# Performance work log

Hardware: AMD Instinct MI355X
Metric: run time of the kernel (lower is better)

Reference implementation:

```python
import jax, jax.numpy as jnp
import numpy as np

EPS = float(np.finfo(np.float32).eps)
B, N, NUM_ATOM, K = 16, 256, 64, 20
NUM_EDGETYPE = 3
SHORT = (1, 2, 3)
LONG = (3, 5, 7)
HIDDEN = (128, 128)
OUT = 1
SCALES = len(SHORT) + len(LONG) + NUM_EDGETYPE + 1  # 10
LB = 1e-4  # lanczos breakdown tolerance


def _xavier(k, fi, fo):
    return jax.random.uniform(k, (fi, fo), jnp.float32, -1.0, 1.0) * (6.0 / (fi + fo)) ** 0.5


def setup_inputs() -> dict:
    key = jax.random.key(0)
    ks = jax.random.split(key, 12)
    inp = {}
    inp["node_feat"] = jax.random.randint(ks[0], (B, N), 0, NUM_ATOM)
    inp["L"] = jax.random.uniform(ks[1], (B, N, N, NUM_EDGETYPE + 1), jnp.float32)
    # embedding_map: Linear(num_atom,1024) -> ReLU -> Linear(1024,num_atom)
    inp["emb_w1"] = _xavier(ks[2], NUM_ATOM, 1024); inp["emb_b1"] = jnp.zeros((1024,), jnp.float32)
    inp["emb_w2"] = _xavier(ks[3], 1024, NUM_ATOM); inp["emb_b2"] = jnp.zeros((NUM_ATOM,), jnp.float32)
    # eigen_map per long scale: Linear(K*K,1024) -> ReLU -> Linear(1024,K*K)
    S, K2 = len(LONG), K * K
    inp["eig_w1"] = jnp.stack([_xavier(jax.random.fold_in(ks[4], i), K2, 1024) for i in range(S)])
    inp["eig_b1"] = jnp.zeros((S, 1024), jnp.float32)
    inp["eig_w2"] = jnp.stack([_xavier(jax.random.fold_in(ks[5], i), 1024, K2) for i in range(S)])
    inp["eig_b2"] = jnp.zeros((S, K2), jnp.float32)
    dims = [NUM_ATOM] + list(HIDDEN) + [OUT]
    inp["filt_w0"] = _xavier(ks[6], dims[0] * SCALES, dims[1]); inp["filt_b0"] = jnp.zeros((dims[1],), jnp.float32)
    inp["filt_w1"] = _xavier(ks[7], dims[1] * SCALES, dims[2]); inp["filt_b1"] = jnp.zeros((dims[2],), jnp.float32)
    inp["filt_wo"] = _xavier(ks[8], dims[2], dims[3]); inp["filt_bo"] = jnp.zeros((dims[3],), jnp.float32)
    inp["att_w"] = _xavier(ks[9], dims[2], 1); inp["att_b"] = jnp.zeros((1,), jnp.float32)
    return inp


def _graph_laplacian(feat, adj_mask):
    # feat: B x N x D; pairwise gaussian affinity, sym-normalized (alpha=0.5)
    diff = feat[:, :, None, :] - feat[:, None, :, :]           # B,N,N,D
    dist2 = jnp.sum(diff * diff, axis=-1).reshape(B, -1)       # B,N*N
    sigma2 = jnp.mean(dist2, axis=1, keepdims=True)
    A = jnp.exp(-dist2 / sigma2).reshape(B, N, N) * adj_mask
    row_sum = jnp.sum(A, axis=2, keepdims=True)
    pad = jnp.where(row_sum == 0.0, 1.0, 0.0)
    D = 1.0 / jnp.sqrt(row_sum + pad)
    return D * A * jnp.swapaxes(D, 1, 2)


def _lanczos(A, key):
    # sequential Lanczos tridiagonalization with double Gram-Schmidt reorth
    q = jax.random.normal(key, (B, N), jnp.float32)
    q = q / jnp.linalg.norm(q, axis=1, keepdims=True)

    def step(carry, i):
        Qbuf, q_prev, qc, beta_prev, valid = carry
        z = jnp.einsum('bij,bj->bi', A, qc)
        alpha = jnp.sum(qc * z, axis=1)
        z = z - alpha[:, None] * qc - beta_prev[:, None] * q_prev
        for _ in range(2):  # reorthogonalize against Q[1..ii-1] (zero cols are no-ops)
            coef = jnp.einsum('bnk,bn->bk', Qbuf, z) / (jnp.sum(Qbuf * Qbuf, axis=1) + EPS)
            z = z - jnp.einsum('bnk,bk->bn', Qbuf, coef)
        beta = jnp.sqrt(jnp.sum(z * z, axis=1))
        valid = valid * (beta >= LB).astype(jnp.float32)
        q_next = z * valid[:, None] / (beta[:, None] + EPS)
        Qbuf = Qbuf.at[:, :, i].set(qc)
        return (Qbuf, qc, q_next, beta, valid), (alpha, beta, valid, qc)

    init = (jnp.zeros((B, N, K), jnp.float32), jnp.zeros((B, N), jnp.float32), q,
            jnp.zeros((B,), jnp.float32), jnp.ones((B,), jnp.float32))
    _, (alphas, betas, valids, qs) = jax.lax.scan(step, init, jnp.arange(K))
    alpha = alphas.T            # B,K
    beta = betas.T              # B,K
    valid = valids.T            # B,K (cumulative 1..1 0..0)
    idx = jnp.sum(valid, axis=1).astype(jnp.int32)   # rank per sample
    alpha = alpha * valid
    beta = beta[:, :K - 1] * valid[:, :K - 1]
    T = jax.vmap(lambda a, b: jnp.diag(a) + jnp.diag(b, 1) + jnp.diag(b, -1))(alpha, beta)
    Q = jnp.transpose(qs, (1, 2, 0))  # B,N,K
    # faithful to source: zero node rows >= idx_mask (only when idx < N)
    row_ok = (jnp.arange(N)[None, :] < idx[:, None]) | (idx[:, None] >= N)
    Q = Q * valid[:, None, :] * row_ok[:, :, None].astype(jnp.float32)
    return T, Q


def _spectral_filters(T, Q, eig_w1, eig_b1, eig_w2, eig_b2, key):
    T_list = []
    TT = T
    b = jax.random.normal(key, (B, K, 1), jnp.float32)
    Tb = b / jnp.linalg.norm(b, axis=1, keepdims=True)
    for ii in range(max(LONG) + 1):
        if ii in LONG:
            T_list.append(TT)
        TT = TT @ T
        # power-iteration cap on spectral radius
        Tb_new = T @ Tb
        l_max = jnp.sum(Tb_new * Tb, axis=1, keepdims=True) / (jnp.sum(Tb * Tb, axis=1, keepdims=True) + EPS)
        TT = TT * (jnp.abs(l_max) <= 1.0).astype(jnp.float32)
        Tb = Tb_new / (jnp.linalg.norm(Tb_new, axis=1, keepdims=True) + EPS)
    triu = jnp.triu(jnp.ones((K, K), jnp.float32))
    eye = jnp.eye(K, dtype=jnp.float32)
    outs = []
    for s in range(len(LONG)):
        h = jax.nn.relu(T_list[s].reshape(B, -1) @ eig_w1[s] + eig_b1[s])
        DD = (h @ eig_w2[s] + eig_b2[s]).reshape(B, K, K)
        DD = DD * triu
        DD = DD + jnp.swapaxes(DD, 1, 2) * (1.0 - eye)  # symmetrize
        outs.append(jnp.einsum('bnk,bkl,bml->bnm', Q, DD, Q))
    return jnp.stack(outs, axis=3)  # B,N,N,S


def reference(node_feat, L, emb_w1, emb_b1, emb_w2, emb_b2, eig_w1, eig_b1, eig_w2, eig_b2,
              filt_w0, filt_b0, filt_w1, filt_b1, filt_wo, filt_bo, att_w, att_b):
    key = jax.random.key(42)
    state = jax.nn.one_hot(node_feat, NUM_ATOM, dtype=jnp.float32)  # frozen identity embedding
    feat = jax.nn.relu(state @ emb_w1 + emb_b1) @ emb_w2 + emb_b2
    Lk = _graph_laplacian(feat, L[:, :, :, 0])
    T, Q = _lanczos(Lk, jax.random.fold_in(key, 0))
    filt_w = (filt_w0, filt_w1)
    filt_b = (filt_b0, filt_b1)
    for tt in range(len(HIDDEN)):
        msg = []
        DD = _spectral_filters(T, Q, eig_w1, eig_b1, eig_w2, eig_b2, jax.random.fold_in(key, tt + 1))
        tmp = state
        for ii in range(1, max(SHORT) + 1):  # short diffusion
            tmp = jnp.einsum('bij,bjd->bid', Lk, tmp)
            if ii in SHORT:
                msg.append(tmp)
        for s in range(len(LONG)):           # long (spectral) diffusion
            msg.append(jnp.einsum('bij,bjd->bid', DD[:, :, :, s], state))
        for e in range(NUM_EDGETYPE + 1):     # per-edgetype propagation
            msg.append(jnp.einsum('bij,bjd->bid', L[:, :, :, e], state))
        msg = jnp.concatenate(msg, axis=2)    # B,N,10*D
        state = jax.nn.relu(msg @ filt_w[tt] + filt_b[tt])
    y = state @ filt_wo + filt_bo             # B,N,1
    att = jax.nn.sigmoid(state @ att_w + att_b)
    score = jnp.mean(att * y, axis=1)          # B,OUT (mask=None -> mean over nodes)
    return score
```

## Files before the change

### kernel.cpp

```cpp
#include <hip/hip_runtime.h>


constexpr int nB = 16;
constexpr int nN = 256;
constexpr int nK = 20;
constexpr int QS = nN + 1;
constexpr float EPSF = 1.1920928955078125e-07f;
constexpr float LBF  = 1e-4f;

#define DEV static __device__ __forceinline__

DEV void tf2x32(unsigned k0, unsigned k1, unsigned x0, unsigned x1,
                unsigned &o0, unsigned &o1) {
  unsigned ks2 = k0 ^ k1 ^ 0x1BD11BDAu;
#define RND(r) { x0 += x1; x1 = (x1 << r) | (x1 >> (32 - r)); x1 ^= x0; }
  x0 += k0;  x1 += k1;
  RND(13) RND(15) RND(26) RND(6)
  x0 += k1;  x1 += ks2 + 1u;
  RND(17) RND(29) RND(16) RND(24)
  x0 += ks2; x1 += k0 + 2u;
  RND(13) RND(15) RND(26) RND(6)
  x0 += k0;  x1 += k1 + 3u;
  RND(17) RND(29) RND(16) RND(24)
  x0 += k1;  x1 += ks2 + 4u;
// ... 91 lines not shown
    float *__restrict__ state0) {
  int g = blockIdx.x;
  int bb = g >> 2, n0 = (g & 3) * 64;
  int t = threadIdx.x;
  int c = t & 63, r4 = t >> 6;
  __shared__ float tl[64][65];
  __shared__ int av[64];
  if (t < 64) av[t] = nf[bb * nN + n0 + t];
  __syncthreads();
  for (int r = r4; r < 64; r += 4) {
    int a = av[r];
    float v = table[(size_t)a * 64 + c];
    tl[r][c] = v;
    feat[((size_t)(bb * nN + n0 + r)) * 64 + c] = v;
    state0[((size_t)(bb * nN + n0 + r)) * 64 + c] = (c == a) ? 1.f : 0.f;
  }
  __syncthreads();
  for (int r = r4; r < 64; r += 4)
    featT[(size_t)bb * 16384 + (size_t)r * nN + n0 + c] = tl[c][r];
}

__global__ __launch_bounds__(256) void dist2_kernel(
    const float *__restrict__ feat, const float *__restrict__ featT,
    float *__restrict__ G, double *__restrict__ part) {
  int g = blockIdx.x;
  int bb = g >> 6, i0 = (g & 63) * 4;
  int t = threadIdx.x;
  __shared__ float fi[4][64];
  __shared__ double s4[4];
  {
    int r = t >> 6, d = t & 63;
    fi[r][d] = feat[((size_t)(bb * nN + i0 + r)) * 64 + d];
  }
  __syncthreads();
  const float *ft = featT + (size_t)bb * 16384 + t;
  float a0 = 0.f, a1 = 0.f, a2 = 0.f, a3 = 0.f;
#pragma unroll 8
  for (int d = 0; d < 64; d++) {
    float x = ft[(size_t)d * nN];
    float d0 = fi[0][d] - x; a0 += d0 * d0;
    float d1 = fi[1][d] - x; a1 += d1 * d1;
    float d2 = fi[2][d] - x; a2 += d2 * d2;
    float d3 = fi[3][d] - x; a3 += d3 * d3;
  }
  size_t base = ((size_t)bb * nN + i0) * nN + t;
  G[base]           = a0;
  G[base + nN]      = a1;
  G[base + 2 * nN]  = a2;
  G[base + 3 * nN]  = a3;
  double tot = blockSumD((double)a0 + (double)a1 + (double)a2 + (double)a3, s4);
  if (t == 0) part[g] = tot;
}

__global__ __launch_bounds__(64) void sigred_kernel(
    const double *__restrict__ part, float *__restrict__ sigma2) {
  int bb = blockIdx.x, t = threadIdx.x;
  double v = part[(size_t)bb * 64 + t];
  v = waveRedD(v);
  if (t == 0) sigma2[bb] = (float)(v / 65536.0);
}

__global__ __launch_bounds__(256) void arow_kernel(
    const float *__restrict__ Lfull, const float *__restrict__ sigma2,
    float *__restrict__ G, float *__restrict__ Dv) {
  int g = blockIdx.x;
  int i = g % nN, bb = g / nN;
  int t = threadIdx.x;
  __shared__ double s4[4];
  float sig = sigma2[bb];
  size_t idx2 = ((size_t)bb * nN + i) * nN + t;
  float a = expf(-G[idx2] / sig) * Lfull[idx2 * 4];
  G[idx2] = a;
  double rs = blockSumD((double)a, s4);
  if (t == 0) {
    float r = (float)rs;
    float pad = (r == 0.f) ? 1.f : 0.f;
    Dv[(size_t)bb * nN + i] = 1.f / sqrtf(r + pad);
  }
}

__global__ __launch_bounds__(256) void lkscale_tr_kernel(
    float *__restrict__ G, const float *__restrict__ Dv,
    float *__restrict__ GT) {
  int g = blockIdx.x;
  int bb = g >> 4, tile = g & 15;
  int ti = (tile >> 2) * 64, tj = (tile & 3) * 64;
  int t = threadIdx.x;
  int lj = t & 63, li0 = t >> 6;
  __shared__ float tl[64][65];
  for (int r = li0; r < 64; r += 4) {
    int i = ti + r;
    size_t idx = ((size_t)bb * nN + i) * nN + tj + lj;
    float v = Dv[(size_t)bb * nN + i] * G[idx] * Dv[(size_t)bb * nN + tj + lj];
    G[idx] = v;
    tl[r][lj] = v;
  }
  __syncthreads();
  for (int r = li0; r < 64; r += 4) {
    int j = tj + r;
    GT[((size_t)bb * nN + j) * nN + ti + lj] = tl[lj][r];
  }
}

__global__ __launch_bounds__(512)
void lanczos_kernel(const float *__restrict__ GT, float *__restrict__ Qout,
                    float *__restrict__ Tout) {
  __shared__ float Qb[nK * QS];
  __shared__ float qc[nN], qp[nN], zz[nN];
  __shared__ double zp[2][nN];
  __shared__ float qn2[nK], sAl[nK], sBe[nK], sVa[nK], coef[nK];
  __shared__ double redA[8], redB[8];
  int bb = blockIdx.x, u = threadIdx.x;
  int t = u & 255, h = u >> 8;
  int wv = u >> 6, lane = u & 63;
  int gid = u >> 4, gl = u & 15;

  const float *Gcol = GT + (size_t)bb * (nN * nN) + (size_t)(h * 128) * nN + t;

  unsigned k0, k1;
  tf2x32(0u, 42u, 0u, 0u, k0, k1);
  float val = 0.f;
  if (h == 0) val = jax_normal(k0, k1, (unsigned)(bb * nN + t));
  {
    double v = waveRedD((double)val * (double)val);
    __syncthreads();
    if (lane == 0) redA[wv] = v;
    __syncthreads();
    double n2 = sum8(redA);
    if (h == 0) {
      qc[t] = val / sqrtf((float)n2);
      qp[t] = 0.f;
    }
  }
  __syncthreads();

  float beta_prev = 0.f, validf = 1.f;

  for (int i = 0; i < nK; i++) {
    double a0 = 0, a1 = 0, a2 = 0, a3 = 0, a4 = 0, a5 = 0, a6 = 0, a7 = 0;
    {
      const float *qv = qc + h * 128;
#pragma unroll
      for (int jj = 0; jj < 128; jj += 8) {
        a0 += (double)Gcol[(size_t)(jj + 0) * nN] * (double)qv[jj + 0];
        a1 += (double)Gcol[(size_t)(jj + 1) * nN] * (double)qv[jj + 1];
        a2 += (double)Gcol[(size_t)(jj + 2) * nN] * (double)qv[jj + 2];
        a3 += (double)Gcol[(size_t)(jj + 3) * nN] * (double)qv[jj + 3];
        a4 += (double)Gcol[(size_t)(jj + 4) * nN] * (double)qv[jj + 4];
        a5 += (double)Gcol[(size_t)(jj + 5) * nN] * (double)qv[jj + 5];
        a6 += (double)Gcol[(size_t)(jj + 6) * nN] * (double)qv[jj + 6];
        a7 += (double)Gcol[(size_t)(jj + 7) * nN] * (double)qv[jj + 7];
      }
    }
    double part = ((a0 + a1) + (a2 + a3)) + ((a4 + a5) + (a6 + a7));
    zp[h][t] = part;
    double apart = (double)qc[t] * part;
    double qpart = (h == 0) ? (double)qc[t] * (double)qc[t] : 0.0;
    apart = waveRedD(apart);
    qpart = waveRedD(qpart);
    if (lane == 0) { redA[wv] = apart; redB[wv] = qpart; }
    __syncthreads();
    float alpha = (float)sum8(redA);
    if (h == 0) {
      float zi = (float)(zp[0][t] + zp[1][t]);
// ... 29 lines not shown
#pragma unroll
      for (int j = 0; j < 16; j++) {
        int n0 = gl + 16 * j;
        p += (double)Qb[gid * QS + n0] * (double)zz[n0];
      }
#pragma unroll
      for (int m = 1; m <= 8; m <<= 1) p += __shfl_xor(p, m, 64);
      if (gl == 0)
        coef[gid] = (float)(p / ((double)qn2[gid] + (double)EPSF));
    }
    __syncthreads();
    double bpart = 0.0;
    if (h == 0) {
      double sub = 0.0;
      for (int k = 0; k < i; k++)
        sub += (double)Qb[k * QS + t] * (double)coef[k];
      float znew = (float)((double)zz[t] - sub);
      zz[t] = znew;
      bpart = (double)znew * (double)znew;
    }
    bpart = waveRedD(bpart);
    if (lane == 0) redA[wv] = bpart;
    __syncthreads();
    float beta = sqrtf((float)sum8(redA));
    validf *= (beta >= LBF) ? 1.f : 0.f;
    if (u == 0) {
      sAl[i] = alpha;
      sBe[i] = beta;
      sVa[i] = validf;
    }
    if (h == 0) {
      float qnext = zz[t] * validf / (beta + EPSF);
      qp[t] = qc[t];
      qc[t] = qnext;
    }
    __syncthreads();
    beta_prev = beta;
  }

  float idxf = 0.f;
  for (int k = 0; k < nK; k++) idxf += sVa[k];
  int idx = (int)idxf;
  if (h == 0) {
    float rowok = ((t < idx) || (idx >= nN)) ? 1.f : 0.f;
    for (int k = 0; k < nK; k++)
      Qout[((size_t)bb * nN + t) * nK + k] = Qb[k * QS + t] * sVa[k] * rowok;
  }
  for (int e = u; e < nK * nK; e += 512) {
    int i = e / nK, j = e % nK;
    float v = 0.f;
    if (i == j) v = sAl[i] * sVa[i];
    else if (j == i + 1) v = sBe[i] * sVa[i];
    else if (i == j + 1) v = sBe[j] * sVa[j];
    Tout[(size_t)bb * nK * nK + e] = v;
  }
}

DEV void spect_body(const float *__restrict__ Tin, float *__restrict__ Tpow2,
                    int bb, int tt, int t, char *smem) {
  float *T_  = (float *)smem;
  float *TT  = T_ + nK * nK;
  float *TTn = TT + nK * nK;
  float *Tb  = TTn + nK * nK;
  float *Tbn = Tb + nK;
  for (int e = t; e < nK * nK; e += 64) {
    float v = Tin[(size_t)bb * nK * nK + e];
    T_[e] = v;
    TT[e] = v;
  }
  unsigned k0, k1;
  tf2x32(0u, 42u, 0u, (unsigned)(tt + 1), k0, k1);
  if (t < nK) Tb[t] = jax_normal(k0, k1, (unsigned)(bb * nK + t));
  __syncthreads();
  float pv = (t < nK) ? Tb[t] * Tb[t] : 0.f;
  float nb = sqrtf(waveRedF(pv));
  if (t < nK) Tb[t] = Tb[t] / nb;
  __syncthreads();
  for (int ii = 0; ii < 8; ii++) {
    if (ii == 3 || ii == 5 || ii == 7) {
      int s = (ii - 3) / 2;
      int sf = tt * 3 + s;
      for (int e = t; e < nK * nK; e += 64)
        Tpow2[((size_t)sf * nB + bb) * nK * nK + e] = TT[e];
    }
    __syncthreads();
    for (int e = t; e < nK * nK; e += 64) {
      int i = e / nK, j = e % nK;
      float a = 0.f;
      for (int l = 0; l < nK; l++) a += TT[i * nK + l] * T_[l * nK + j];
      TTn[e] = a;
    }
    if (t < nK) {
      float a = 0.f;
      for (int l = 0; l < nK; l++) a += T_[t * nK + l] * Tb[l];
      Tbn[t] = a;
    }
    __syncthreads();
    float pn = (t < nK) ? Tbn[t] * Tb[t] : 0.f;
    float pd = (t < nK) ? Tb[t] * Tb[t] : 0.f;
    float num = waveRedF(pn);
    float den = waveRedF(pd);
    float lmax = num / (den + EPSF);
    float keep = (fabsf(lmax) <= 1.0f) ? 1.f : 0.f;
    __syncthreads();
    for (int e = t; e < nK * nK; e += 64) TT[e] = TTn[e] * keep;
    float p2 = (t < nK) ? Tbn[t] * Tbn[t] : 0.f;
    float nn = sqrtf(waveRedF(p2));
    if (t < nK) Tb[t] = Tbn[t] / (nn + EPSF);
    __syncthreads();
  }
}

DEV void eig1_body(const float *__restrict__ Tpow2, const float *__restrict__ w1p,
                   const float *__restrict__ b1p, float *__restrict__ h2,
                   int g, int t, char *smem) {
  int oc = g & 15, sf = g >> 4;
  int sw = sf % 3;
  int o = (t & 63) + oc * 64, bbg = t >> 6;
  float *tp = (float *)smem;
  for (int e = t; e < nB * 400; e += 256)
    tp[e] = Tpow2[(size_t)sf * nB * 400 + e];
  __syncthreads();
  float bias = b1p[(size_t)sw * 1024 + o];
  float acc0 = bias, acc1 = bias, acc2 = bias, acc3 = bias;
  const float *W = w1p + (size_t)sw * 400 * 1024 + o;
  const float *t0 = tp + (bbg + 0) * 400;
  const float *t1 = tp + (bbg + 4) * 400;
  const float *t2 = tp + (bbg + 8) * 400;
  const float *t3 = tp + (bbg + 12) * 400;
  for (int k = 0; k < 400; k++) {
    float w = W[(size_t)k * 1024];
    acc0 += t0[k] * w;
    acc1 += t1[k] * w;
    acc2 += t2[k] * w;
    acc3 += t3[k] * w;
  }
  h2[((size_t)sf * nB + (bbg + 0))  * 1024 + o] = fmaxf(acc0, 0.f);
  h2[((size_t)sf * nB + (bbg + 4))  * 1024 + o] = fmaxf(acc1, 0.f);
  h2[((size_t)sf * nB + (bbg + 8))  * 1024 + o] = fmaxf(acc2, 0.f);
  h2[((size_t)sf * nB + (bbg + 12)) * 1024 + o] = fmaxf(acc3, 0.f);
}

DEV void eig2_body(const float *__restrict__ h2, const float *__restrict__ w2p,
                   const float *__restrict__ b2p, float *__restrict__ raw2,
                   int g, int t, char *smem) {
  int kc = g % 25, sf = g / 25;
  int sw = sf % 3;
  int kl = (t & 15) + kc * 16, bb = t >> 4;
  float *hh = (float *)smem;
  for (int e = t; e < nB * 1024; e += 256)
    hh[(e >> 10) * 1025 + (e & 1023)] = h2[(size_t)sf * nB * 1024 + e];
  __syncthreads();
  float acc = b2p[(size_t)sw * 400 + kl];
  const float *W = w2p + (size_t)sw * 1024 * 400 + kl;
  const float *hv = hh + bb * 1025;
  for (int o = 0; o < 1024; o++) acc += hv[o] * W[(size_t)o * 400];
  raw2[((size_t)sf * nB + bb) * 400 + kl] = acc;
}

DEV void qtstate_body(const float *__restrict__ Q, const float *__restrict__ state,
                      float *__restrict__ E, int g, int t, int Din, char *smem) {
  int k = g % nK, bb = g / nK;
  float *qcol = (float *)smem;
  for (int n = t; n < nN; n += Din)
    qcol[n] = Q[((size_t)bb * nN + n) * nK + k];
  __syncthreads();
  const float *st = state + (size_t)bb * nN * Din;
  float acc = 0.f;
  for (int n = 0; n < nN; n++) acc += qcol[n] * st[(size_t)n * Din + t];
  E[((size_t)bb * nK + k) * Din + t] = acc;
}

DEV void lk_body(const float *__restrict__ Lk, const float *__restrict__ in,
                 int inStride, float *__restrict__ out, int outStride,
                 int g, int t, int Din, char *smem) {
  int bb = g >> 5, r0 = (g & 31) * 8;
  float (*rows)[nN] = (float (*)[nN])smem;
  for (int e = t; e < 8 * nN; e += Din) {
    int r = e >> 8, j = e & 255;
    rows[r][j] = Lk[((size_t)bb * nN + r0 + r) * nN + j];
  }
  __syncthreads();
  float acc[8] = {0.f, 0.f, 0.f, 0.f, 0.f, 0.f, 0.f, 0.f};
  const float *ip = in + (size_t)bb * nN * inStride + t;
  for (int j = 0; j < nN; j++) {
    float x = ip[(size_t)j * inStride];
#pragma unroll
    for (int r = 0; r < 8; r++) acc[r] += rows[r][j] * x;
  }
#pragma unroll
  for (int r = 0; r < 8; r++)
    out[((size_t)bb * nN + r0 + r) * outStride + t] = acc[r];
}

DEV void edgemsg_body(const float *__restrict__ Lfull,
                      const float *__restrict__ state, float *__restrict__ msg,
                      int C, int g, int t, int Din, char *smem) {
  int bb = g >> 6, r0 = (g & 63) * 4;
  float4 (*rows4)[nN] = (float4 (*)[nN])smem;
  const float4 *L4 = (const float4 *)Lfull;
  for (int e = t; e < 4 * nN; e += Din) {
    int r = e >> 8, j = e & 255;
    rows4[r][j] = L4[((size_t)bb * nN + r0 + r) * nN + j];
  }
  __syncthreads();
  float acc[4][4];
#pragma unroll
  for (int r = 0; r < 4; r++)
#pragma unroll
    for (int e = 0; e < 4; e++) acc[r][e] = 0.f;
  const float *st = state + (size_t)bb * nN * Din + t;
  for (int j = 0; j < nN; j++) {
    float x = st[(size_t)j * Din];
#pragma unroll
    for (int r = 0; r < 4; r++) {
      float4 lv = rows4[r][j];
      acc[r][0] += lv.x * x;
      acc[r][1] += lv.y * x;
      acc[r][2] += lv.z * x;
      acc[r][3] += lv.w * x;
    }
  }
#pragma unroll
  for (int r = 0; r < 4; r++)
#pragma unroll
    for (int e = 0; e < 4; e++)
      msg[((size_t)bb * nN + r0 + r) * C + (6 + e) * Din + t] = acc[r][e];
}

DEV void ddE_body(const float *__restrict__ raw, const float *__restrict__ E,
                  float *__restrict__ F, int g, int t, int Din, char *smem) {
  int k = g % nK, bb = (g / nK) % nB, s = g / (nK * nB);
  float *dr = (float *)smem;
  if (t < nK) {
    int mi = k < t ? k : t, ma = k < t ? t : k;
    dr[t] = raw[((size_t)s * nB + bb) * 400 + mi * nK + ma];
  }
  __syncthreads();
  float acc = 0.f;
  for (int l = 0; l < nK; l++)
    acc += dr[l] * E[((size_t)bb * nK + l) * Din + t];
  F[(((size_t)s * nB + bb) * nK + k) * Din + t] = acc;
}

DEV void longmsg_body(const float *__restrict__ Q, const float *__restrict__ F,
                      float *__restrict__ msg, int C, int g, int t, int Din,
                      char *smem) {
  int i = g % nN, bb = g / nN;
  float *qr = (float *)smem;
  if (t < nK) qr[t] = Q[((size_t)bb * nN + i) * nK + t];
  __syncthreads();
  for (int s = 0; s < 3; s++) {
    float acc = 0.f;
    for (int k = 0; k < nK; k++)
      acc += qr[k] * F[(((size_t)s * nB + bb) * nK + k) * Din + t];
    msg[((size_t)bb * nN + i) * C + (3 + s) * Din + t] = acc;
  }
}

__global__ __launch_bounds__(64) void l1d1_spect_kernel(
    const float *__restrict__ T, float *__restrict__ Tpow2) {
  __shared__ __align__(16) char smem[5120];
  int bb = blockIdx.x & 15, tt = blockIdx.x >> 4;
  spect_body(T, Tpow2, bb, tt, threadIdx.x, smem);
}

__global__ void msgD1_kernel(const float *__restrict__ Q,
                             const float *__restrict__ state,
                             float *__restrict__ E,
                             const float *__restrict__ Lk,
                             float *__restrict__ msg,
                             const float *__restrict__ Lfull, int C) {
  __shared__ __align__(16) char smem[16384];
  int t = threadIdx.x, Din = blockDim.x;
  int gb = blockIdx.x;
  if (gb < nB * nK) {
    qtstate_body(Q, state, E, gb, t, Din, smem);
  } else if (gb < nB * nK + nB * nN / 8) {
    lk_body(Lk, state, Din, msg + 0 * Din, C, gb - nB * nK, t, Din, smem);
  } else {
    edgemsg_body(Lfull, state, msg, C, gb - nB * nK - nB * nN / 8, t, Din, smem);
  }
}

__global__ __launch_bounds__(256) void l1d2_kernel(
    const float *__restrict__ Tpow2, const float *__restrict__ w1p,
    const float *__restrict__ b1p, float *__restrict__ h2,
    const float *__restrict__ Lk, float *__restrict__ msg, int C) {
  __shared__ __align__(16) char smem[26240];
  int t = threadIdx.x;
  int gb = blockIdx.x;
  if (gb < 96) {
    eig1_body(Tpow2, w1p, b1p, h2, gb, t, smem);
  } else {
    int g = gb - 96;
    int bb = g >> 5, r0 = (g & 31) * 8;
    float (*rows)[nN] = (float (*)[nN])smem;
    for (int e = t; e < 8 * nN; e += 256) {
      int r = e >> 8, j = e & 255;
      rows[r][j] = Lk[((size_t)bb * nN + r0 + r) * nN + j];
    }
    __syncthreads();
    if (t < 64) {
      float acc[8] = {0.f, 0.f, 0.f, 0.f, 0.f, 0.f, 0.f, 0.f};
      const float *ip = msg + (size_t)bb * nN * C + 0 * 64 + t;
      for (int j = 0; j < nN; j++) {
        float x = ip[(size_t)j * C];
#pragma unroll
        for (int r = 0; r < 8; r++) acc[r] += rows[r][j] * x;
      }
#pragma unroll
      for (int r = 0; r < 8; r++)
        msg[((size_t)bb * nN + r0 + r) * C + 1 * 64 + t] = acc[r];
    }
  }
}

__global__ __launch_bounds__(256) void l1d3_kernel(
    const float *__restrict__ h2, const float *__restrict__ w2p,
    const float *__restrict__ b2p, float *__restrict__ raw2,
    const float *__restrict__ Lk, float *__restrict__ msg, int C) {
  __shared__ __align__(16) char smem[65600];
  int t = threadIdx.x;
  int gb = blockIdx.x;
  if (gb < 150) {
    eig2_body(h2, w2p, b2p, raw2, gb, t, smem);
  } else {
    int g = gb - 150;
    int bb = g >> 5, r0 = (g & 31) * 8;
    float (*rows)[nN] = (float (*)[nN])smem;
    for (int e = t; e < 8 * nN; e += 256) {
      int r = e >> 8, j = e & 255;
      rows[r][j] = Lk[((size_t)bb * nN + r0 + r) * nN + j];
    }
    __syncthreads();
    if (t < 64) {
      float acc[8] = {0.f, 0.f, 0.f, 0.f, 0.f, 0.f, 0.f, 0.f};
      const float *ip = msg + (size_t)bb * nN * C + 1 * 64 + t;
      for (int j = 0; j < nN; j++) {
        float x = ip[(size_t)j * C];
#pragma unroll
        for (int r = 0; r < 8; r++) acc[r] += rows[r][j] * x;
      }
#pragma unroll
      for (int r = 0; r < 8; r++)
        msg[((size_t)bb * nN + r0 + r) * C + 2 * 64 + t] = acc[r];
    }
  }
}

__global__ void msgD2_kernel(const float *__restrict__ raw,
                             const float *__restrict__ E,
                             float *__restrict__ F,
                             const float *__restrict__ Lk,
                             float *__restrict__ msg, int C, int withLk) {
  __shared__ __align__(16) char smem[8192];
  int t = threadIdx.x, Din = blockDim.x;
  int gb = blockIdx.x;
  if (gb < 3 * nB * nK) {
    ddE_body(raw, E, F, gb, t, Din, smem);
  } else {
    lk_body(Lk, msg + 0 * Din, C, msg + 1 * Din, C, gb - 3 * nB * nK, t, Din,
            smem);
  }
}

__global__ void msgD3_kernel(const float *__restrict__ Q,
                             const float *__restrict__ F,
                             const float *__restrict__ Lk,
                             float *__restrict__ msg, int C) {
  __shared__ __align__(16) char smem[8192];
  int t = threadIdx.x, Din = blockDim.x;
  int gb = blockIdx.x;
  if (gb < nB * nN) {
    longmsg_body(Q, F, msg, C, gb, t, Din, smem);
  } else {
    lk_body(Lk, msg + 1 * Din, C, msg + 2 * Din, C, gb - nB * nN, t, Din, smem);
  }
}

__global__ __launch_bounds__(256) void filt_kernel(
    const float *__restrict__ msg, const float *__restrict__ W,
    const float *__restrict__ bias, float *__restrict__ out, int C) {
  int g = blockIdx.x;
  int base = g * 16;
  int t = threadIdx.x;
  int o = t & 127, ih = t >> 7;
  __shared__ float mt[16][64];
  __shared__ float wt[64][128];
  float acc[8];
  float bo = bias[o];
#pragma unroll
  for (int r = 0; r < 8; r++) acc[r] = bo;
  for (int c0 = 0; c0 < C; c0 += 64) {
    __syncthreads();
    for (int e = t; e < 16 * 64; e += 256) {
      int r = e >> 6, c = e & 63;
      mt[r][c] = msg[((size_t)(base + r)) * C + c0 + c];
    }
    for (int e = t; e < 64 * 128; e += 256)
      wt[e >> 7][e & 127] = W[(size_t)(c0 + (e >> 7)) * 128 + (e & 127)];
    __syncthreads();
    for (int c = 0; c < 64; c++) {
      float w = wt[c][o];
#pragma unroll
      for (int r = 0; r < 8; r++) acc[r] += mt[ih * 8 + r][c] * w;
    }
  }
#pragma unroll
  for (int r = 0; r < 8; r++)
    out[((size_t)(base + ih * 8 + r)) * 128 + o] = fmaxf(acc[r], 0.f);
}

__global__ __launch_bounds__(256) void score_kernel(
    const float *__restrict__ state, const float *__restrict__ wo,
    const float *__restrict__ bo, const float *__restrict__ aw,
    const float *__restrict__ ab, float *__restrict__ out) {
  __shared__ float sl[64 * 129];
  __shared__ double s4[4];
  int bb = blockIdx.x, t = threadIdx.x;
  float bof = bo[0], abf = ab[0];
  double dsum = 0.0;
  for (int r0 = 0; r0 < nN; r0 += 64) {
    __syncthreads();
    for (int e = t; e < 64 * 128; e += 256) {
      int r = e >> 7, o = e & 127;
      sl[r * 129 + o] = state[((size_t)bb * nN + r0 + r) * 128 + o];
    }
    __syncthreads();
    if (t < 64) {
      const float *sr = sl + t * 129;
// ... 1 lines not shown
      for (int o = 0; o < 128; o++) {
        float v = sr[o];
        sy += v * wo[o];
        sa += v * aw[o];
      }
      float att = 1.f / (1.f + expf(-sa));
      dsum += (double)(att * sy);
    }
  }
  double m = blockSumD(dsum, s4);
  if (t == 0) out[bb] = (float)(m / (double)nN);
}

extern "C" void kernel_launch(void *const *d_in, const int *in_sizes, int n_in,
                              void *d_out, int out_size, void *d_ws,
                              size_t ws_size, hipStream_t stream) {
  (void)in_sizes; (void)n_in; (void)out_size;
  const int   *node_feat = (const int *)d_in[0];
  const float *Lfull     = (const float *)d_in[1];
  const float *emb_w1    = (const float *)d_in[2];
  const float *emb_b1    = (const float *)d_in[3];
  const float *emb_w2    = (const float *)d_in[4];
  const float *emb_b2    = (const float *)d_in[5];
  const float *eig_w1    = (const float *)d_in[6];
  const float *eig_b1    = (const float *)d_in[7];
  const float *eig_w2    = (const float *)d_in[8];
  const float *eig_b2    = (const float *)d_in[9];
  const float *filt_w0   = (const float *)d_in[10];
  const float *filt_b0   = (const float *)d_in[11];
  const float *filt_w1   = (const float *)d_in[12];
  const float *filt_b1   = (const float *)d_in[13];
  const float *filt_wo   = (const float *)d_in[14];
  const float *filt_bo   = (const float *)d_in[15];
  const float *att_w     = (const float *)d_in[16];
  const float *att_b     = (const float *)d_in[17];

  float *ws   = (float *)d_ws;
  float *G    = ws;
  float *msg  = G + 1048576;
  float *st0  = msg + 5242880;
  float *st1  = st0 + 262144;
  float *st2  = st1 + 524288;
  float *feat = st2 + 524288;
  float *table= feat + 262144;
  float *Q    = table + 4096;
  float *T    = Q + 81920;
  float *Tpow = T + 6400;
  float *DD   = Tpow + 19200;
  float *h    = DD + 19200;
  float *E    = h + 49152;
  float *F    = E + 40960;
  float *Dv   = F + 122880;
  double *part   = (double *)(Dv + 4096);
  float  *sigma2 = (float *)(part + nB * nN);
  float *GT    = msg;
  float *featT = msg + 1048576;
  float *Tpow2 = feat;
  float *raw2  = feat + 38400;
  float *h2    = feat + 76800;
  const size_t needBytes = (size_t)(8220432) * 4;
  if (ws_size < needBytes) return;

  feat_table_kernel<<<64, 256, 0, stream>>>(emb_w1, emb_b1, emb_w2, emb_b2, table);
  feat_state_tr_kernel<<<nB * 4, 256, 0, stream>>>(node_feat, table, feat,
                                                   featT, st0);
  dist2_kernel<<<nB * 64, 256, 0, stream>>>(feat, featT, G, part);
  sigred_kernel<<<nB, 64, 0, stream>>>(part, sigma2);
  arow_kernel<<<nB * nN, 256, 0, stream>>>(Lfull, sigma2, G, Dv);
  lkscale_tr_kernel<<<nB * 16, 256, 0, stream>>>(G, Dv, GT);
  lanczos_kernel<<<nB, 512, 0, stream>>>(GT, Q, T);

  const int QTB = nB * nK;
  const int LKB = nB * nN / 8;
  const int EDB = nB * nN / 4;
  const int DDB = 3 * nB * nK;
  const int LMB = nB * nN;

  {
    int Din = 64, C = 640;
    const float *rawT = raw2;
    l1d1_spect_kernel<<<nB * 2, 64, 0, stream>>>(T, Tpow2);
    msgD1_kernel<<<QTB + LKB + EDB, Din, 0, stream>>>(Q, st0, E, G, msg,
                                                      Lfull, C);
    l1d2_kernel<<<96 + LKB, 256, 0, stream>>>(Tpow2, eig_w1, eig_b1, h2, G,
                                              msg, C);
    l1d3_kernel<<<150 + LKB, 256, 0, stream>>>(h2, eig_w2, eig_b2, raw2, G,
                                               msg, C);
    msgD2_kernel<<<DDB, Din, 0, stream>>>(rawT, E, F, G, msg, C, 0);
    msgD3_kernel<<<LMB, Din, 0, stream>>>(Q, F, G, msg, C);
    filt_kernel<<<nB * nN / 16, 256, 0, stream>>>(msg, filt_w0, filt_b0, st1, C);
  }
  {
    int Din = 128, C = 1280;
    const float *rawT = raw2 + (size_t)3 * nB * 400;
    msgD1_kernel<<<QTB + LKB + EDB, Din, 0, stream>>>(Q, st1, E, G, msg,
                                                      Lfull, C);
    msgD2_kernel<<<DDB + LKB, Din, 0, stream>>>(rawT, E, F, G, msg, C, 1);
    msgD3_kernel<<<LMB + LKB, Din, 0, stream>>>(Q, F, G, msg, C);
    filt_kernel<<<nB * nN / 16, 256, 0, stream>>>(msg, filt_w1, filt_b1, st2, C);
  }
  score_kernel<<<nB, 256, 0, stream>>>(st2, filt_wo, filt_bo, att_w, att_b,
                                       (float *)d_out);
}
```

Before: 632.0 us.

## Fuse spectral power loop into Lanczos and merge long-diffusion stages

Folds the sigma reduction into the affinity-row kernel and moves the spectral power iteration into the tail of the Lanczos kernel. This removes two launches. It also fuses the per-scale DD·E and Q·F steps into one block-tiled kernel that keeps the intermediate F in shared memory. The remaining short-diffusion and eigen-MLP work is regrouped into fewer combined launches per layer. The main cost targeted is launch count and the global round-trips for F. In exchange there are serial 20x20 matmuls on the 16 Lanczos blocks and larger shared memory use, which may reduce occupancy.

```diff
diff --git a/kernel.cpp b/kernel.cpp
--- a/kernel.cpp
+++ b/kernel.cpp
@@ -167,22 +167,21 @@
   if (t == 0) part[g] = tot;
 }
 
-__global__ __launch_bounds__(64) void sigred_kernel(
-    const double *__restrict__ part, float *__restrict__ sigma2) {
-  int bb = blockIdx.x, t = threadIdx.x;
-  double v = part[(size_t)bb * 64 + t];
-  v = waveRedD(v);
-  if (t == 0) sigma2[bb] = (float)(v / 65536.0);
-}
-
 __global__ __launch_bounds__(256) void arow_kernel(
-    const float *__restrict__ Lfull, const float *__restrict__ sigma2,
+    const float *__restrict__ Lfull, const double *__restrict__ part,
     float *__restrict__ G, float *__restrict__ Dv) {
   int g = blockIdx.x;
   int i = g % nN, bb = g / nN;
   int t = threadIdx.x;
   __shared__ double s4[4];
-  float sig = sigma2[bb];
+  __shared__ float ssig;
+  if (t < 64) {
+    double v = part[(size_t)bb * 64 + t];
+    v = waveRedD(v);
+    if (t == 0) ssig = (float)(v / 65536.0);
+  }
+  __syncthreads();
+  float sig = ssig;
   size_t idx2 = ((size_t)bb * nN + i) * nN + t;
   float a = expf(-G[idx2] / sig) * Lfull[idx2 * 4];
   G[idx2] = a;
@@ -219,12 +218,14 @@
 
 __global__ __launch_bounds__(512)
 void lanczos_kernel(const float *__restrict__ GT, float *__restrict__ Qout,
-                    float *__restrict__ Tout) {
+                    float *__restrict__ Tpow2) {
   __shared__ float Qb[nK * QS];
   __shared__ float qc[nN], qp[nN], zz[nN];
   __shared__ double zp[2][nN];
   __shared__ float qn2[nK], sAl[nK], sBe[nK], sVa[nK], coef[nK];
   __shared__ double redA[8], redB[8];
+  __shared__ float sT[400], sTT[400], sTTn[400], sTb[nK], sTbn[nK];
+  __shared__ float sKeep;
   int bb = blockIdx.x, u = threadIdx.x;
   int t = u & 255, h = u >> 8;
   int wv = u >> 6, lane = u & 63;
@@ -360,93 +361,157 @@
     if (i == j) v = sAl[i] * sVa[i];
     else if (j == i + 1) v = sBe[i] * sVa[i];
     else if (i == j + 1) v = sBe[j] * sVa[j];
-    Tout[(size_t)bb * nK * nK + e] = v;
-  }
-}
-
-DEV void spect_body(const float *__restrict__ Tin, float *__restrict__ Tpow2,
-                    int bb, int tt, int t, char *smem) {
-  float *T_  = (float *)smem;
-  float *TT  = T_ + nK * nK;
-  float *TTn = TT + nK * nK;
-  float *Tb  = TTn + nK * nK;
-  float *Tbn = Tb + nK;
-  for (int e = t; e < nK * nK; e += 64) {
-    float v = Tin[(size_t)bb * nK * nK + e];
-    T_[e] = v;
-    TT[e] = v;
-  }
-  unsigned k0, k1;
-  tf2x32(0u, 42u, 0u, (unsigned)(tt + 1), k0, k1);
-  if (t < nK) Tb[t] = jax_normal(k0, k1, (unsigned)(bb * nK + t));
-  __syncthreads();
-  float pv = (t < nK) ? Tb[t] * Tb[t] : 0.f;
-  float nb = sqrtf(waveRedF(pv));
-  if (t < nK) Tb[t] = Tb[t] / nb;
-  __syncthreads();
-  for (int ii = 0; ii < 8; ii++) {
-    if (ii == 3 || ii == 5 || ii == 7) {
-      int s = (ii - 3) / 2;
-      int sf = tt * 3 + s;
-      for (int e = t; e < nK * nK; e += 64)
-        Tpow2[((size_t)sf * nB + bb) * nK * nK + e] = TT[e];
-    }
-    __syncthreads();
-    for (int e = t; e < nK * nK; e += 64) {
-      int i = e / nK, j = e % nK;
-      float a = 0.f;
-      for (int l = 0; l < nK; l++) a += TT[i * nK + l] * T_[l * nK + j];
-      TTn[e] = a;
-    }
-    if (t < nK) {
-      float a = 0.f;
-      for (int l = 0; l < nK; l++) a += T_[t * nK + l] * Tb[l];
-      Tbn[t] = a;
-    }
-    __syncthreads();
-    float pn = (t < nK) ? Tbn[t] * Tb[t] : 0.f;
-    float pd = (t < nK) ? Tb[t] * Tb[t] : 0.f;
-    float num = waveRedF(pn);
-    float den = waveRedF(pd);
-    float lmax = num / (den + EPSF);
-    float keep = (fabsf(lmax) <= 1.0f) ? 1.f : 0.f;
-    __syncthreads();
-    for (int e = t; e < nK * nK; e += 64) TT[e] = TTn[e] * keep;
-    float p2 = (t < nK) ? Tbn[t] * Tbn[t] : 0.f;
-    float nn = sqrtf(waveRedF(p2));
-    if (t < nK) Tb[t] = Tbn[t] / (nn + EPSF);
-    __syncthreads();
-  }
-}
-
-DEV void eig1_body(const float *__restrict__ Tpow2, const float *__restrict__ w1p,
-                   const float *__restrict__ b1p, float *__restrict__ h2,
-                   int g, int t, char *smem) {
+    sT[e] = v;
+  }
+  __syncthreads();
+
+  for (int tt = 0; tt < 2; tt++) {
+    for (int e = u; e < nK * nK; e += 512) sTT[e] = sT[e];
+    if (u < 64) {
+      unsigned kk0, kk1;
+      tf2x32(0u, 42u, 0u, (unsigned)(tt + 1), kk0, kk1);
+      float tb = (u < nK) ? jax_normal(kk0, kk1, (unsigned)(bb * nK + u)) : 0.f;
+      float pv = (u < nK) ? tb * tb : 0.f;
+      float nb = sqrtf(waveRedF(pv));
+      if (u < nK) sTb[u] = tb / nb;
+    }
+    __syncthreads();
+    for (int ii = 0; ii < 8; ii++) {
+      if (ii == 3 || ii == 5 || ii == 7) {
+        int s = (ii - 3) / 2;
+        int sf = tt * 3 + s;
+        for (int e = u; e < nK * nK; e += 512)
+          Tpow2[((size_t)sf * nB + bb) * nK * nK + e] = sTT[e];
+      }
+      __syncthreads();
+      for (int e = u; e < nK * nK; e += 512) {
+        int i = e / nK, j = e % nK;
+        float a = 0.f;
+        for (int l = 0; l < nK; l++) a += sTT[i * nK + l] * sT[l * nK + j];
+        sTTn[e] = a;
+      }
+      if (u < nK) {
+        float a = 0.f;
+        for (int l = 0; l < nK; l++) a += sT[u * nK + l] * sTb[l];
+        sTbn[u] = a;
+      }
+      __syncthreads();
+      if (u < 64) {
+        float pn = (u < nK) ? sTbn[u] * sTb[u] : 0.f;
+        float pd = (u < nK) ? sTb[u] * sTb[u] : 0.f;
+        float num = waveRedF(pn);
+        float den = waveRedF(pd);
+        float lmax = num / (den + EPSF);
+        if (u == 0) sKeep = (fabsf(lmax) <= 1.0f) ? 1.f : 0.f;
+      }
+      __syncthreads();
+      float keep = sKeep;
+      for (int e = u; e < nK * nK; e += 512) sTT[e] = sTTn[e] * keep;
+      if (u < 64) {
+        float p2 = (u < nK) ? sTbn[u] * sTbn[u] : 0.f;
+        float nn = sqrtf(waveRedF(p2));
+        if (u < nK) sTb[u] = sTbn[u] / (nn + EPSF);
+      }
+      __syncthreads();
+    }
+    __syncthreads();
+  }
+}
+
+DEV void qtstate_body(const float *__restrict__ Q, const float *__restrict__ state,
+                      float *__restrict__ E, int g, int t, int Din, char *smem) {
+  int k = g % nK, bb = g / nK;
+  float *qcol = (float *)smem;
+  for (int n = t; n < nN; n += Din)
+    qcol[n] = Q[((size_t)bb * nN + n) * nK + k];
+  __syncthreads();
+  const float *st = state + (size_t)bb * nN * Din;
+  float acc = 0.f;
+  for (int n = 0; n < nN; n++) acc += qcol[n] * st[(size_t)n * Din + t];
+  E[((size_t)bb * nK + k) * Din + t] = acc;
+}
+
+DEV void lk_body(const float *__restrict__ Lk, const float *__restrict__ in,
+                 int inStride, float *__restrict__ out, int outStride,
+                 int g, int t, int Din, char *smem) {
+  int bb = g >> 5, r0 = (g & 31) * 8;
+  float (*rows)[nN] = (float (*)[nN])smem;
+  for (int e = t; e < 8 * nN; e += Din) {
+    int r = e >> 8, j = e & 255;
+    rows[r][j] = Lk[((size_t)bb * nN + r0 + r) * nN + j];
+  }
+  __syncthreads();
+  float acc[8] = {0.f, 0.f, 0.f, 0.f, 0.f, 0.f, 0.f, 0.f};
+  const float *ip = in + (size_t)bb * nN * inStride + t;
+  for (int j = 0; j < nN; j++) {
+    float x = ip[(size_t)j * inStride];
+#pragma unroll
+    for (int r = 0; r < 8; r++) acc[r] += rows[r][j] * x;
+  }
+#pragma unroll
+  for (int r = 0; r < 8; r++)
+    out[((size_t)bb * nN + r0 + r) * outStride + t] = acc[r];
+}
+
+DEV void edgemsg_body(const float *__restrict__ Lfull,
+                      const float *__restrict__ state, float *__restrict__ msg,
+                      int C, int g, int t, int Din, char *smem) {
+  int bb = g >> 6, r0 = (g & 63) * 4;
+  float4 (*rows4)[nN] = (float4 (*)[nN])smem;
+  const float4 *L4 = (const float4 *)Lfull;
+  for (int e = t; e < 4 * nN; e += Din) {
+    int r = e >> 8, j = e & 255;
+    rows4[r][j] = L4[((size_t)bb * nN + r0 + r) * nN + j];
+  }
+  __syncthreads();
+  float acc[4][4];
+#pragma unroll
+  for (int r = 0; r < 4; r++)
+#pragma unroll
+    for (int e = 0; e < 4; e++) acc[r][e] = 0.f;
+  const float *st = state + (size_t)bb * nN * Din + t;
+  for (int j = 0; j < nN; j++) {
+    float x = st[(size_t)j * Din];
+#pragma unroll
+    for (int r = 0; r < 4; r++) {
+      float4 lv = rows4[r][j];
+      acc[r][0] += lv.x * x;
+      acc[r][1] += lv.y * x;
+      acc[r][2] += lv.z * x;
+      acc[r][3] += lv.w * x;
+    }
+  }
+#pragma unroll
+  for (int r = 0; r < 4; r++)
+#pragma unroll
+    for (int e = 0; e < 4; e++)
+      msg[((size_t)bb * nN + r0 + r) * C + (6 + e) * Din + t] = acc[r][e];
+}
+
+DEV void eig1_body64(const float *__restrict__ Tpow2,
+                     const float *__restrict__ w1p,
+                     const float *__restrict__ b1p, float *__restrict__ h2,
+                     int g, int t, char *smem) {
   int oc = g & 15, sf = g >> 4;
   int sw = sf % 3;
-  int o = (t & 63) + oc * 64, bbg = t >> 6;
+  int o = t + oc * 64;
   float *tp = (float *)smem;
-  for (int e = t; e < nB * 400; e += 256)
+  for (int e = t; e < nB * 400; e += 64)
     tp[e] = Tpow2[(size_t)sf * nB * 400 + e];
   __syncthreads();
   float bias = b1p[(size_t)sw * 1024 + o];
-  float acc0 = bias, acc1 = bias, acc2 = bias, acc3 = bias;
+  float acc[16];
+#pragma unroll
+  for (int b2 = 0; b2 < 16; b2++) acc[b2] = bias;
   const float *W = w1p + (size_t)sw * 400 * 1024 + o;
-  const float *t0 = tp + (bbg + 0) * 400;
-  const float *t1 = tp + (bbg + 4) * 400;
-  const float *t2 = tp + (bbg + 8) * 400;
-  const float *t3 = tp + (bbg + 12) * 400;
   for (int k = 0; k < 400; k++) {
     float w = W[(size_t)k * 1024];
-    acc0 += t0[k] * w;
-    acc1 += t1[k] * w;
-    acc2 += t2[k] * w;
-    acc3 += t3[k] * w;
-  }
-  h2[((size_t)sf * nB + (bbg + 0))  * 1024 + o] = fmaxf(acc0, 0.f);
-  h2[((size_t)sf * nB + (bbg + 4))  * 1024 + o] = fmaxf(acc1, 0.f);
-  h2[((size_t)sf * nB + (bbg + 8))  * 1024 + o] = fmaxf(acc2, 0.f);
-  h2[((size_t)sf * nB + (bbg + 12)) * 1024 + o] = fmaxf(acc3, 0.f);
+#pragma unroll
+    for (int b2 = 0; b2 < 16; b2++) acc[b2] += tp[b2 * 400 + k] * w;
+  }
+#pragma unroll
+  for (int b2 = 0; b2 < 16; b2++)
+    h2[((size_t)sf * nB + b2) * 1024 + o] = fmaxf(acc[b2], 0.f);
 }
 
 DEV void eig2_body(const float *__restrict__ h2, const float *__restrict__ w2p,
@@ -466,165 +531,60 @@
   raw2[((size_t)sf * nB + bb) * 400 + kl] = acc;
 }
 
-DEV void qtstate_body(const float *__restrict__ Q, const float *__restrict__ state,
-                      float *__restrict__ E, int g, int t, int Din, char *smem) {
-  int k = g % nK, bb = g / nK;
-  float *qcol = (float *)smem;
-  for (int n = t; n < nN; n += Din)
-    qcol[n] = Q[((size_t)bb * nN + n) * nK + k];
-  __syncthreads();
-  const float *st = state + (size_t)bb * nN * Din;
-  float acc = 0.f;
-  for (int n = 0; n < nN; n++) acc += qcol[n] * st[(size_t)n * Din + t];
-  E[((size_t)bb * nK + k) * Din + t] = acc;
-}
-
-DEV void lk_body(const float *__restrict__ Lk, const float *__restrict__ in,
-                 int inStride, float *__restrict__ out, int outStride,
-                 int g, int t, int Din, char *smem) {
-  int bb = g >> 5, r0 = (g & 31) * 8;
-  float (*rows)[nN] = (float (*)[nN])smem;
-  for (int e = t; e < 8 * nN; e += Din) {
-    int r = e >> 8, j = e & 255;
-    rows[r][j] = Lk[((size_t)bb * nN + r0 + r) * nN + j];
-  }
-  __syncthreads();
-  float acc[8] = {0.f, 0.f, 0.f, 0.f, 0.f, 0.f, 0.f, 0.f};
-  const float *ip = in + (size_t)bb * nN * inStride + t;
-  for (int j = 0; j < nN; j++) {
-    float x = ip[(size_t)j * inStride];
-#pragma unroll
-    for (int r = 0; r < 8; r++) acc[r] += rows[r][j] * x;
-  }
-#pragma unroll
-  for (int r = 0; r < 8; r++)
-    out[((size_t)bb * nN + r0 + r) * outStride + t] = acc[r];
-}
-
-DEV void edgemsg_body(const float *__restrict__ Lfull,
-                      const float *__restrict__ state, float *__restrict__ msg,
-                      int C, int g, int t, int Din, char *smem) {
-  int bb = g >> 6, r0 = (g & 63) * 4;
-  float4 (*rows4)[nN] = (float4 (*)[nN])smem;
-  const float4 *L4 = (const float4 *)Lfull;
-  for (int e = t; e < 4 * nN; e += Din) {
-    int r = e >> 8, j = e & 255;
-    rows4[r][j] = L4[((size_t)bb * nN + r0 + r) * nN + j];
-  }
-  __syncthreads();
-  float acc[4][4];
-#pragma unroll
-  for (int r = 0; r < 4; r++)
-#pragma unroll
-    for (int e = 0; e < 4; e++) acc[r][e] = 0.f;
-  const float *st = state + (size_t)bb * nN * Din + t;
-  for (int j = 0; j < nN; j++) {
-    float x = st[(size_t)j * Din];
-#pragma unroll
-    for (int r = 0; r < 4; r++) {
-      float4 lv = rows4[r][j];
-      acc[r][0] += lv.x * x;
-      acc[r][1] += lv.y * x;
-      acc[r][2] += lv.z * x;
-      acc[r][3] += lv.w * x;
-    }
-  }
-#pragma unroll
-  for (int r = 0; r < 4; r++)
-#pragma unroll
-    for (int e = 0; e < 4; e++)
-      msg[((size_t)bb * nN + r0 + r) * C + (6 + e) * Din + t] = acc[r][e];
-}
-
-DEV void ddE_body(const float *__restrict__ raw, const float *__restrict__ E,
-                  float *__restrict__ F, int g, int t, int Din, char *smem) {
-  int k = g % nK, bb = (g / nK) % nB, s = g / (nK * nB);
-  float *dr = (float *)smem;
-  if (t < nK) {
-    int mi = k < t ? k : t, ma = k < t ? t : k;
-    dr[t] = raw[((size_t)s * nB + bb) * 400 + mi * nK + ma];
-  }
-  __syncthreads();
-  float acc = 0.f;
+DEV void dlm_body(const float *__restrict__ raw, const float *__restrict__ E,
+                  const float *__restrict__ Q, float *__restrict__ msg,
+                  int C, int g, int t, int Din, char *smem) {
+  int bb = g >> 4, i0 = (g & 15) * 16;
+  float *Es = (float *)smem;
+  float *Fs = Es + nK * Din;
+  float *Qs = Fs + 3 * nK * Din;
   for (int l = 0; l < nK; l++)
-    acc += dr[l] * E[((size_t)bb * nK + l) * Din + t];
-  F[(((size_t)s * nB + bb) * nK + k) * Din + t] = acc;
-}
-
-DEV void longmsg_body(const float *__restrict__ Q, const float *__restrict__ F,
-                      float *__restrict__ msg, int C, int g, int t, int Din,
-                      char *smem) {
-  int i = g % nN, bb = g / nN;
-  float *qr = (float *)smem;
-  if (t < nK) qr[t] = Q[((size_t)bb * nN + i) * nK + t];
-  __syncthreads();
-  for (int s = 0; s < 3; s++) {
+    Es[l * Din + t] = E[((size_t)bb * nK + l) * Din + t];
+  for (int e = t; e < 16 * nK; e += Din)
+    Qs[e] = Q[((size_t)bb * nN + i0 + e / nK) * nK + (e % nK)];
+  __syncthreads();
+  for (int sk = 0; sk < 3 * nK; sk++) {
+    int s = sk / nK, k = sk % nK;
+    const float *rp = raw + ((size_t)s * nB + bb) * 400;
     float acc = 0.f;
-    for (int k = 0; k < nK; k++)
-      acc += qr[k] * F[(((size_t)s * nB + bb) * nK + k) * Din + t];
-    msg[((size_t)bb * nN + i) * C + (3 + s) * Din + t] = acc;
-  }
-}
-
-__global__ __launch_bounds__(64) void l1d1_spect_kernel(
-    const float *__restrict__ T, float *__restrict__ Tpow2) {
-  __shared__ __align__(16) char smem[5120];
-  int bb = blockIdx.x & 15, tt = blockIdx.x >> 4;
-  spect_body(T, Tpow2, bb, tt, threadIdx.x, smem);
-}
-
-__global__ void msgD1_kernel(const float *__restrict__ Q,
-                             const float *__restrict__ state,
-                             float *__restrict__ E,
-                             const float *__restrict__ Lk,
-                             float *__restrict__ msg,
-                             const float *__restrict__ Lfull, int C) {
-  __shared__ __align__(16) char smem[16384];
-  int t = threadIdx.x, Din = blockDim.x;
+    for (int l = 0; l < nK; l++) {
+      int mi = k < l ? k : l, ma = k < l ? l : k;
+      acc += rp[mi * nK + ma] * Es[l * Din + t];
+    }
+    Fs[sk * Din + t] = acc;
+  }
+  for (int r = 0; r < 16; r++) {
+    const float *qr = Qs + r * nK;
+    for (int s = 0; s < 3; s++) {
+      float acc = 0.f;
+      for (int k = 0; k < nK; k++)
+        acc += qr[k] * Fs[(s * nK + k) * Din + t];
+      msg[((size_t)bb * nN + i0 + r) * C + (3 + s) * Din + t] = acc;
+    }
+  }
+}
+
+__global__ __launch_bounds__(64) void l1d1_kernel(
+    const float *__restrict__ Q, const float *__restrict__ state,
+    float *__restrict__ E, const float *__restrict__ Lk,
+    float *__restrict__ msg, const float *__restrict__ Lfull,
+    const float *__restrict__ Tpow2, const float *__restrict__ w1p,
+    const float *__restrict__ b1p, float *__restrict__ h2, int C) {
+  __shared__ __align__(16) char smem[26240];
+  int t = threadIdx.x;
   int gb = blockIdx.x;
-  if (gb < nB * nK) {
-    qtstate_body(Q, state, E, gb, t, Din, smem);
-  } else if (gb < nB * nK + nB * nN / 8) {
-    lk_body(Lk, state, Din, msg + 0 * Din, C, gb - nB * nK, t, Din, smem);
+  if (gb < 320) {
+    qtstate_body(Q, state, E, gb, t, 64, smem);
+  } else if (gb < 320 + 512) {
+    lk_body(Lk, state, 64, msg + 0 * 64, C, gb - 320, t, 64, smem);
+  } else if (gb < 320 + 512 + 1024) {
+    edgemsg_body(Lfull, state, msg, C, gb - 832, t, 64, smem);
   } else {
-    edgemsg_body(Lfull, state, msg, C, gb - nB * nK - nB * nN / 8, t, Din, smem);
+    eig1_body64(Tpow2, w1p, b1p, h2, gb - 1856, t, smem);
   }
 }
 
 __global__ __launch_bounds__(256) void l1d2_kernel(
-    const float *__restrict__ Tpow2, const float *__restrict__ w1p,
-    const float *__restrict__ b1p, float *__restrict__ h2,
-    const float *__restrict__ Lk, float *__restrict__ msg, int C) {
-  __shared__ __align__(16) char smem[26240];
-  int t = threadIdx.x;
-  int gb = blockIdx.x;
-  if (gb < 96) {
-    eig1_body(Tpow2, w1p, b1p, h2, gb, t, smem);
-  } else {
-    int g = gb - 96;
-    int bb = g >> 5, r0 = (g & 31) * 8;
-    float (*rows)[nN] = (float (*)[nN])smem;
-    for (int e = t; e < 8 * nN; e += 256) {
-      int r = e >> 8, j = e & 255;
-      rows[r][j] = Lk[((size_t)bb * nN + r0 + r) * nN + j];
-    }
-    __syncthreads();
-    if (t < 64) {
-      float acc[8] = {0.f, 0.f, 0.f, 0.f, 0.f, 0.f, 0.f, 0.f};
-      const float *ip = msg + (size_t)bb * nN * C + 0 * 64 + t;
-      for (int j = 0; j < nN; j++) {
-        float x = ip[(size_t)j * C];
-#pragma unroll
-        for (int r = 0; r < 8; r++) acc[r] += rows[r][j] * x;
-      }
-#pragma unroll
-      for (int r = 0; r < 8; r++)
-        msg[((size_t)bb * nN + r0 + r) * C + 1 * 64 + t] = acc[r];
-    }
-  }
-}
-
-__global__ __launch_bounds__(256) void l1d3_kernel(
     const float *__restrict__ h2, const float *__restrict__ w2p,
     const float *__restrict__ b2p, float *__restrict__ raw2,
     const float *__restrict__ Lk, float *__restrict__ msg, int C) {
@@ -644,7 +604,7 @@
     __syncthreads();
     if (t < 64) {
       float acc[8] = {0.f, 0.f, 0.f, 0.f, 0.f, 0.f, 0.f, 0.f};
-      const float *ip = msg + (size_t)bb * nN * C + 1 * 64 + t;
+      const float *ip = msg + (size_t)bb * nN * C + 0 * 64 + t;
       for (int j = 0; j < nN; j++) {
         float x = ip[(size_t)j * C];
 #pragma unroll
@@ -652,39 +612,60 @@
       }
 #pragma unroll
       for (int r = 0; r < 8; r++)
-        msg[((size_t)bb * nN + r0 + r) * C + 2 * 64 + t] = acc[r];
-    }
-  }
-}
-
-__global__ void msgD2_kernel(const float *__restrict__ raw,
-                             const float *__restrict__ E,
-                             float *__restrict__ F,
-                             const float *__restrict__ Lk,
-                             float *__restrict__ msg, int C, int withLk) {
+        msg[((size_t)bb * nN + r0 + r) * C + 1 * 64 + t] = acc[r];
+    }
+  }
+}
+
+__global__ __launch_bounds__(64) void l1d3_kernel(
+    const float *__restrict__ raw, const float *__restrict__ E,
+    const float *__restrict__ Q, const float *__restrict__ Lk,
+    float *__restrict__ msg, int C) {
+  __shared__ __align__(16) char smem[22016];
+  int t = threadIdx.x;
+  int gb = blockIdx.x;
+  if (gb < 256) {
+    dlm_body(raw, E, Q, msg, C, gb, t, 64, smem);
+  } else {
+    lk_body(Lk, msg + 1 * 64, C, msg + 2 * 64, C, gb - 256, t, 64, smem);
+  }
+}
+
+__global__ __launch_bounds__(128) void l2d1_kernel(
+    const float *__restrict__ Q, const float *__restrict__ state,
+    float *__restrict__ E, const float *__restrict__ Lk,
+    float *__restrict__ msg, const float *__restrict__ Lfull, int C) {
+  __shared__ __align__(16) char smem[16384];
+  int t = threadIdx.x;
+  int gb = blockIdx.x;
+  if (gb < 320) {
+    qtstate_body(Q, state, E, gb, t, 128, smem);
+  } else if (gb < 832) {
+    lk_body(Lk, state, 128, msg + 0 * 128, C, gb - 320, t, 128, smem);
+  } else {
+    edgemsg_body(Lfull, state, msg, C, gb - 832, t, 128, smem);
+  }
+}
+
+__global__ __launch_bounds__(128) void l2d2_kernel(
+    const float *__restrict__ raw, const float *__restrict__ E,
+    const float *__restrict__ Q, const float *__restrict__ Lk,
+    float *__restrict__ msg, int C) {
+  __shared__ __align__(16) char smem[43328];
+  int t = threadIdx.x;
+  int gb = blockIdx.x;
+  if (gb < 256) {
+    dlm_body(raw, E, Q, msg, C, gb, t, 128, smem);
+  } else {
+    lk_body(Lk, msg + 0 * 128, C, msg + 1 * 128, C, gb - 256, t, 128, smem);
+  }
+}
+
+__global__ __launch_bounds__(128) void l2d3_kernel(
+    const float *__restrict__ Lk, float *__restrict__ msg, int C) {
   __shared__ __align__(16) char smem[8192];
-  int t = threadIdx.x, Din = blockDim.x;
-  int gb = blockIdx.x;
-  if (gb < 3 * nB * nK) {
-    ddE_body(raw, E, F, gb, t, Din, smem);
-  } else {
-    lk_body(Lk, msg + 0 * Din, C, msg + 1 * Din, C, gb - 3 * nB * nK, t, Din,
-            smem);
-  }
-}
-
-__global__ void msgD3_kernel(const float *__restrict__ Q,
-                             const float *__restrict__ F,
-                             const float *__restrict__ Lk,
-                             float *__restrict__ msg, int C) {
-  __shared__ __align__(16) char smem[8192];
-  int t = threadIdx.x, Din = blockDim.x;
-  int gb = blockIdx.x;
-  if (gb < nB * nN) {
-    longmsg_body(Q, F, msg, C, gb, t, Din, smem);
-  } else {
-    lk_body(Lk, msg + 1 * Din, C, msg + 2 * Din, C, gb - nB * nN, t, Din, smem);
-  }
+  lk_body(Lk, msg + 1 * 128, C, msg + 2 * 128, C, blockIdx.x, threadIdx.x, 128,
+          smem);
 }
 
 __global__ __launch_bounds__(256) void filt_kernel(
@@ -792,7 +773,6 @@
   float *F    = E + 40960;
   float *Dv   = F + 122880;
   double *part   = (double *)(Dv + 4096);
-  float  *sigma2 = (float *)(part + nB * nN);
   float *GT    = msg;
   float *featT = msg + 1048576;
   float *Tpow2 = feat;
@@ -805,38 +785,27 @@
   feat_state_tr_kernel<<<nB * 4, 256, 0, stream>>>(node_feat, table, feat,
                                                    featT, st0);
   dist2_kernel<<<nB * 64, 256, 0, stream>>>(feat, featT, G, part);
-  sigred_kernel<<<nB, 64, 0, stream>>>(part, sigma2);
-  arow_kernel<<<nB * nN, 256, 0, stream>>>(Lfull, sigma2, G, Dv);
+  arow_kernel<<<nB * nN, 256, 0, stream>>>(Lfull, part, G, Dv);
   lkscale_tr_kernel<<<nB * 16, 256, 0, stream>>>(G, Dv, GT);
-  lanczos_kernel<<<nB, 512, 0, stream>>>(GT, Q, T);
-
-  const int QTB = nB * nK;
-  const int LKB = nB * nN / 8;
-  const int EDB = nB * nN / 4;
-  const int DDB = 3 * nB * nK;
-  const int LMB = nB * nN;
+  lanczos_kernel<<<nB, 512, 0, stream>>>(GT, Q, Tpow2);
 
   {
-    int Din = 64, C = 640;
+    int C = 640;
     const float *rawT = raw2;
-    l1d1_spect_kernel<<<nB * 2, 64, 0, stream>>>(T, Tpow2);
-    msgD1_kernel<<<QTB + LKB + EDB, Din, 0, stream>>>(Q, st0, E, G, msg,
+    l1d1_kernel<<<320 + 512 + 1024 + 96, 64, 0, stream>>>(
+        Q, st0, E, G, msg, Lfull, Tpow2, eig_w1, eig_b1, h2, C);
+    l1d2_kernel<<<150 + 512, 256, 0, stream>>>(h2, eig_w2, eig_b2, raw2, G,
+                                               msg, C);
+    l1d3_kernel<<<256 + 512, 64, 0, stream>>>(rawT, E, Q, G, msg, C);
+    filt_kernel<<<nB * nN / 16, 256, 0, stream>>>(msg, filt_w0, filt_b0, st1, C);
+  }
+  {
+    int C = 1280;
+    const float *rawT = raw2 + (size_t)3 * nB * 400;
+    l2d1_kernel<<<320 + 512 + 1024, 128, 0, stream>>>(Q, st1, E, G, msg,
                                                       Lfull, C);
-    l1d2_kernel<<<96 + LKB, 256, 0, stream>>>(Tpow2, eig_w1, eig_b1, h2, G,
-                                              msg, C);
-    l1d3_kernel<<<150 + LKB, 256, 0, stream>>>(h2, eig_w2, eig_b2, raw2, G,
-                                               msg, C);
-    msgD2_kernel<<<DDB, Din, 0, stream>>>(rawT, E, F, G, msg, C, 0);
-    msgD3_kernel<<<LMB, Din, 0, stream>>>(Q, F, G, msg, C);
-    filt_kernel<<<nB * nN / 16, 256, 0, stream>>>(msg, filt_w0, filt_b0, st1, C);
-  }
-  {
-    int Din = 128, C = 1280;
-    const float *rawT = raw2 + (size_t)3 * nB * 400;
-    msgD1_kernel<<<QTB + LKB + EDB, Din, 0, stream>>>(Q, st1, E, G, msg,
-                                                      Lfull, C);
-    msgD2_kernel<<<DDB + LKB, Din, 0, stream>>>(rawT, E, F, G, msg, C, 1);
-    msgD3_kernel<<<LMB + LKB, Din, 0, stream>>>(Q, F, G, msg, C);
+    l2d2_kernel<<<256 + 512, 128, 0, stream>>>(rawT, E, Q, G, msg, C);
+    l2d3_kernel<<<512, 128, 0, stream>>>(G, msg, C);
     filt_kernel<<<nB * nN / 16, 256, 0, stream>>>(msg, filt_w1, filt_b1, st2, C);
   }
   score_kernel<<<nB, 256, 0, stream>>>(st2, filt_wo, filt_bo, att_w, att_b,
```

Measured after the change: 712.2 us. 12.7% more time.
